# Kernel optimization log

Hardware: AMD Instinct MI355X
Metric: run time of the kernel (lower is better)

The kernel has to match this reference:

```python
import jax, jax.numpy as jnp
import numpy as np

TOPK = 2
SCALE = 32.0 / 16.0  # alpha / rank
EPS = 1e-20


def setup_inputs() -> dict:
    key = jax.random.key(0)
    ks = jax.random.split(key, 6)
    B, S, D = 4, 4096, 2048
    E, R, QO, VO = 8, 16, 2048, 2048
    return {
        "hidden_states": jax.random.normal(ks[0], (B, S, D), dtype=jnp.float32),
        "router_weight": jax.random.normal(ks[1], (E, D), dtype=jnp.float32) * 0.02,
        "q_lora_a": jax.random.normal(ks[2], (E, D, R), dtype=jnp.float32) * 0.02,
        "q_lora_b": jax.random.normal(ks[3], (E, R, QO), dtype=jnp.float32) * 0.02,
        "v_lora_a": jax.random.normal(ks[4], (E, D, R), dtype=jnp.float32) * 0.02,
        "v_lora_b": jax.random.normal(ks[5], (E, R, VO), dtype=jnp.float32) * 0.02,
    }


def reference(hidden_states, router_weight, q_lora_a, q_lora_b, v_lora_a, v_lora_b):
    orig_shape = hidden_states.shape[:-1]
    D = hidden_states.shape[-1]
    E = router_weight.shape[0]
    h = hidden_states.reshape(-1, D)                       # [T, D]

    # --- routing ---
    logits = h @ router_weight.T                           # [T, E]
    probs = jax.nn.softmax(logits, axis=-1)
    scores, idx = jax.lax.top_k(probs, TOPK)               # [T, K]
    scores = scores / (jnp.sum(scores, axis=-1, keepdims=True) + EPS)
    # dense per-expert combine weight (0 for unselected experts), incl. LoRA scale
    w = jnp.sum(jax.nn.one_hot(idx, E, dtype=h.dtype) * scores[..., None], axis=1) * SCALE  # [T, E]

    # --- grouped LoRA (dense over experts; E and rank are small) ---
    q_low = jnp.einsum('td,edr->ter', h, q_lora_a) * w[:, :, None]  # [T, E, R]
    v_low = jnp.einsum('td,edr->ter', h, v_lora_a) * w[:, :, None]
    q_delta = jnp.einsum('ter,erq->tq', q_low, q_lora_b)            # [T, QO]
    v_delta = jnp.einsum('ter,erv->tv', v_low, v_lora_b)            # [T, VO]

    return (q_delta.reshape(*orig_shape, q_delta.shape[-1]),
            v_delta.reshape(*orig_shape, v_delta.shape[-1]))
```

## Files before the change

### kernel.cpp

```cpp
#include <hip/hip_runtime.h>

#define T_TOKENS 16384
#define DIM 2048
#define NE 8
#define QOUT 2048
#define LSCALE 2.0f

typedef __attribute__((ext_vector_type(4))) float f32x4;
typedef __attribute__((ext_vector_type(8))) short s16x8;
typedef __attribute__((ext_vector_type(4))) short s16x4;

__device__ __forceinline__ short f2bf(float f) {
  unsigned u = __builtin_bit_cast(unsigned, f);
  u += 0x7fffu + ((u >> 16) & 1u);
  return (short)(u >> 16);
}

__global__ __launch_bounds__(256) void k_pack(
    const float* __restrict__ qa, const float* __restrict__ qb,
    const float* __restrict__ va, const float* __restrict__ vb,
    short* __restrict__ Bq1, short* __restrict__ Bv1,
    short* __restrict__ Bq2, short* __restrict__ Bv2) {
  int tid = blockIdx.x * 256 + threadIdx.x;
  if (tid < 65536) {
    int mat = tid >> 15;
    int idx = tid & 32767;
    int d8 = idx >> 7, c = idx & 127;
    int e = c >> 4, r = c & 15;
    const float* src = mat ? va : qa;
    short* dst = mat ? Bv1 : Bq1;
    s16x8 v;
#pragma unroll
    for (int j = 0; j < 8; ++j)
      v[j] = f2bf(src[((size_t)e * DIM + d8 * 8 + j) * 16 + r]);
    *(s16x8*)(dst + (size_t)idx * 8) = v;
  } else {
    int t2 = tid - 65536;
    int mat = t2 >> 15;
    int idx = t2 & 32767;
    int k8 = idx >> 11, c = idx & 2047;
    const float* src = mat ? vb : qb;
    short* dst = mat ? Bv2 : Bq2;
    s16x8 v;
#pragma unroll
    for (int j = 0; j < 8; ++j)
      v[j] = f2bf(src[(size_t)(k8 * 8 + j) * QOUT + c]);
    *(s16x8*)(dst + (size_t)idx * 8) = v;
  }
}

__global__ __launch_bounds__(256) void k_s1(
    const float* __restrict__ h, const float* __restrict__ rw,
    const short* __restrict__ Bq1, const short* __restrict__ Bv1,
    short* __restrict__ lowq, short* __restrict__ lowv) {
  __shared__ float rwl[NE * DIM];
  __shared__ short At[2][32][40];
  __shared__ float wl[32][NE];

  const int tid = threadIdx.x;
  const int lane = tid & 63, wv = tid >> 6;
  const int lrow = lane & 15, lk = lane >> 4;
  const int row0 = blockIdx.x * 32;
  const int c0 = wv * 64;
  const int r = tid >> 3;
  const int kq = (tid & 7) * 4;

  {
    const float4* src = (const float4*)rw;
    float4* dst = (float4*)rwl;
#pragma unroll
    for (int i = 0; i < 16; ++i) dst[tid + i * 256] = src[tid + i * 256];
  }
  __syncthreads();

  float lg[NE] = {0.f, 0.f, 0.f, 0.f, 0.f, 0.f, 0.f, 0.f};
  f32x4 acc[2][4] = {};
  int cur = 0;
  const float* hrow = h + (size_t)(row0 + r) * DIM + kq;

  for (int kb = 0; kb < DIM; kb += 32) {
    float4 hv = *(const float4*)(hrow + kb);
#pragma unroll
    for (int e = 0; e < NE; ++e) {
      float4 rv = *(const float4*)&rwl[e * DIM + kb + kq];
      lg[e] += hv.x * rv.x + hv.y * rv.y + hv.z * rv.z + hv.w * rv.w;
    }
    s16x4 hb4;
    hb4[0] = f2bf(hv.x); hb4[1] = f2bf(hv.y);
    hb4[2] = f2bf(hv.z); hb4[3] = f2bf(hv.w);
    *(s16x4*)&At[cur][r][kq] = hb4;
    s16x8 b[4];
#pragma unroll
    for (int ct = 0; ct < 4; ++ct) {
      int c = c0 + ct * 16 + lrow;
      int cc = c & 127;
      const short* bp = (c < 128) ? Bq1 : Bv1;
      b[ct] = *(const s16x8*)(bp + ((size_t)((kb >> 3) + lk) * 128 + cc) * 8);
    }
    __syncthreads();
    s16x8 a[2];
#pragma unroll
    for (int rt = 0; rt < 2; ++rt)
      a[rt] = *(const s16x8*)&At[cur][rt * 16 + lrow][lk * 8];
#pragma unroll
    for (int rt = 0; rt < 2; ++rt)
#pragma unroll
      for (int ct = 0; ct < 4; ++ct)
        acc[rt][ct] = __builtin_amdgcn_mfma_f32_16x16x32_bf16(b[ct], a[rt], acc[rt][ct], 0, 0, 0);
    cur ^= 1;
  }

#pragma unroll
  for (int e = 0; e < NE; ++e) {
    lg[e] += __shfl_xor(lg[e], 1, 64);
    lg[e] += __shfl_xor(lg[e], 2, 64);
    lg[e] += __shfl_xor(lg[e], 4, 64);
  }
  float mx = lg[0];
#pragma unroll
  for (int e = 1; e < NE; ++e) mx = fmaxf(mx, lg[e]);
  float p[NE], sum = 0.f;
#pragma unroll
  for (int e = 0; e < NE; ++e) { p[e] = expf(lg[e] - mx); sum += p[e]; }
  int i1 = 0; float v1 = p[0];
#pragma unroll
  for (int e = 1; e < NE; ++e) if (p[e] > v1) { v1 = p[e]; i1 = e; }
  float v2 = -1.f; int i2 = 0;
#pragma unroll
  for (int e = 0; e < NE; ++e) if (e != i1 && p[e] > v2) { v2 = p[e]; i2 = e; }
  float s1 = v1 / sum, s2 = v2 / sum;
  float dn = s1 + s2 + 1e-20f;
  float w1 = s1 / dn * LSCALE, w2 = s2 / dn * LSCALE;
  int el = tid & 7;
  wl[r][el] = (el == i1) ? w1 : ((el == i2) ? w2 : 0.f);
  __syncthreads();

#pragma unroll
  for (int rt = 0; rt < 2; ++rt)
#pragma unroll
    for (int ct = 0; ct < 4; ++ct) {
      int t = row0 + rt * 16 + lrow;
      int col = c0 + ct * 16 + lk * 4;
      int cc = col & 127;
      int e = cc >> 4;
      short* op = (col < 128) ? lowq : lowv;
      float wgt = wl[rt * 16 + lrow][e];
      s16x4 v;
#pragma unroll
      for (int j = 0; j < 4; ++j) v[j] = f2bf(acc[rt][ct][j] * wgt);
      *(s16x4*)(op + (size_t)t * 128 + cc) = v;
    }
}

__global__ __launch_bounds__(256) void k_up(
    const short* __restrict__ lowq, const short* __restrict__ lowv,
    const short* __restrict__ Bq2, const short* __restrict__ Bv2,
    float* __restrict__ out) {
  const int lane = threadIdx.x & 63, wv = threadIdx.x >> 6;
  const int lrow = lane & 15, lk = lane >> 4;
  const int row0 = blockIdx.x * 64;
  const int m = blockIdx.y >> 1;
  const int half = blockIdx.y & 1;
  const short* low = m ? lowv : lowq;
  const short* B = m ? Bv2 : Bq2;
  float* op = out + (size_t)m * T_TOKENS * QOUT;

  s16x8 a[4][4];
#pragma unroll
  for (int rt = 0; rt < 4; ++rt)
#pragma unroll
    for (int kk = 0; kk < 4; ++kk)
      a[rt][kk] = *(const s16x8*)(low + (size_t)(row0 + rt * 16 + lrow) * 128 + kk * 32 + lk * 8);

#pragma unroll
  for (int sub = 0; sub < 4; ++sub) {
    int cb = half * 1024 + sub * 256 + wv * 64;
    f32x4 acc[4][4] = {};
#pragma unroll
    for (int kk = 0; kk < 4; ++kk) {
      s16x8 b[4];
#pragma unroll
      for (int ct = 0; ct < 4; ++ct) {
        int c = cb + ct * 16 + lrow;
        b[ct] = *(const s16x8*)(B + ((size_t)(kk * 4 + lk) * QOUT + c) * 8);
      }
#pragma unroll
      for (int rt = 0; rt < 4; ++rt)
#pragma unroll
        for (int ct = 0; ct < 4; ++ct)
          acc[rt][ct] = __builtin_amdgcn_mfma_f32_16x16x32_bf16(b[ct], a[rt][kk], acc[rt][ct], 0, 0, 0);
    }
#pragma unroll
    for (int rt = 0; rt < 4; ++rt)
#pragma unroll
      for (int ct = 0; ct < 4; ++ct) {
        int t = row0 + rt * 16 + lrow;
        int col = cb + ct * 16 + lk * 4;
        *(f32x4*)(op + (size_t)t * QOUT + col) = acc[rt][ct];
      }
  }
}

extern "C" void kernel_launch(void* const* d_in, const int* in_sizes, int n_in,
                              void* d_out, int out_size, void* d_ws, size_t ws_size,
                              hipStream_t stream) {
  const float* h  = (const float*)d_in[0];
  const float* rw = (const float*)d_in[1];
  const float* qa = (const float*)d_in[2];
  const float* qb = (const float*)d_in[3];
  const float* va = (const float*)d_in[4];
  const float* vb = (const float*)d_in[5];
  float* out = (float*)d_out;
  char* ws = (char*)d_ws;

  short* Bq1 = (short*)(ws);
  short* Bv1 = (short*)(ws + (512 << 10));
  short* Bq2 = (short*)(ws + (1024 << 10));
  short* Bv2 = (short*)(ws + (1536 << 10));
  short* lowq = (short*)(ws + (2 << 20));
  short* lowv = (short*)(ws + (6 << 20));

  k_pack<<<512, 256, 0, stream>>>(qa, qb, va, vb, Bq1, Bv1, Bq2, Bv2);
  k_s1<<<T_TOKENS / 32, 256, 0, stream>>>(h, rw, Bq1, Bv1, lowq, lowv);
  dim3 g2(T_TOKENS / 64, 4);
  k_up<<<g2, 256, 0, stream>>>(lowq, lowv, Bq2, Bv2, out);
}
```

Baseline: 155.7 us.

## Prefetch next k-slice in s1, double tokens per block, tune k_up occupancy

The stage-1 kernel now processes 64 tokens per 512-thread block, so the router weights staged in LDS are reused across twice as many rows. Each iteration register-prefetches the next hidden-state and B1 fragments before the current MFMAs, and the full __syncthreads is replaced by an LDS-only waitcnt plus barrier. k_up gets a min-blocks-per-CU launch bound. The aim is to hide global-load latency and amortize the router-weight copy, at the cost of more registers and fewer resident blocks.

```diff
diff --git a/kernel.cpp b/kernel.cpp
--- a/kernel.cpp
+++ b/kernel.cpp
@@ -14,6 +14,11 @@
   unsigned u = __builtin_bit_cast(unsigned, f);
   u += 0x7fffu + ((u >> 16) & 1u);
   return (short)(u >> 16);
+}
+
+__device__ __forceinline__ void barrier_lds() {
+  asm volatile("s_waitcnt lgkmcnt(0)" ::: "memory");
+  __builtin_amdgcn_s_barrier();
 }
 
 __global__ __launch_bounds__(256) void k_pack(
@@ -49,19 +54,20 @@
   }
 }
 
-__global__ __launch_bounds__(256) void k_s1(
+__global__ __launch_bounds__(512, 4) void k_s1(
     const float* __restrict__ h, const float* __restrict__ rw,
     const short* __restrict__ Bq1, const short* __restrict__ Bv1,
     short* __restrict__ lowq, short* __restrict__ lowv) {
   __shared__ float rwl[NE * DIM];
-  __shared__ short At[2][32][40];
-  __shared__ float wl[32][NE];
+  __shared__ short At[2][64][40];
+  __shared__ float wl[64][NE];
 
   const int tid = threadIdx.x;
   const int lane = tid & 63, wv = tid >> 6;
   const int lrow = lane & 15, lk = lane >> 4;
-  const int row0 = blockIdx.x * 32;
-  const int c0 = wv * 64;
+  const int row0 = blockIdx.x * 64;
+  const int rh = wv >> 2;
+  const int c0 = (wv & 3) * 64;
   const int r = tid >> 3;
   const int kq = (tid & 7) * 4;
 
@@ -69,17 +75,36 @@
     const float4* src = (const float4*)rw;
     float4* dst = (float4*)rwl;
 #pragma unroll
-    for (int i = 0; i < 16; ++i) dst[tid + i * 256] = src[tid + i * 256];
+    for (int i = 0; i < 8; ++i) dst[tid + i * 512] = src[tid + i * 512];
   }
   __syncthreads();
+
+  const float* hrow = h + (size_t)(row0 + r) * DIM;
+  const short* bp[4]; int cc4[4];
+#pragma unroll
+  for (int ct = 0; ct < 4; ++ct) {
+    int c = c0 + ct * 16 + lrow;
+    bp[ct] = (c < 128) ? Bq1 : Bv1;
+    cc4[ct] = c & 127;
+  }
+
+  float4 hv = *(const float4*)(hrow + kq);
+  s16x8 b[4];
+#pragma unroll
+  for (int ct = 0; ct < 4; ++ct)
+    b[ct] = *(const s16x8*)(bp[ct] + ((size_t)lk * 128 + cc4[ct]) * 8);
 
   float lg[NE] = {0.f, 0.f, 0.f, 0.f, 0.f, 0.f, 0.f, 0.f};
   f32x4 acc[2][4] = {};
   int cur = 0;
-  const float* hrow = h + (size_t)(row0 + r) * DIM + kq;
 
   for (int kb = 0; kb < DIM; kb += 32) {
-    float4 hv = *(const float4*)(hrow + kb);
+    const int kn = (kb + 32) & (DIM - 1);
+    float4 hvn = *(const float4*)(hrow + kn + kq);
+    s16x8 bn[4];
+#pragma unroll
+    for (int ct = 0; ct < 4; ++ct)
+      bn[ct] = *(const s16x8*)(bp[ct] + ((size_t)((kn >> 3) + lk) * 128 + cc4[ct]) * 8);
 #pragma unroll
     for (int e = 0; e < NE; ++e) {
       float4 rv = *(const float4*)&rwl[e * DIM + kb + kq];
@@ -89,24 +114,19 @@
     hb4[0] = f2bf(hv.x); hb4[1] = f2bf(hv.y);
     hb4[2] = f2bf(hv.z); hb4[3] = f2bf(hv.w);
     *(s16x4*)&At[cur][r][kq] = hb4;
-    s16x8 b[4];
-#pragma unroll
-    for (int ct = 0; ct < 4; ++ct) {
-      int c = c0 + ct * 16 + lrow;
-      int cc = c & 127;
-      const short* bp = (c < 128) ? Bq1 : Bv1;
-      b[ct] = *(const s16x8*)(bp + ((size_t)((kb >> 3) + lk) * 128 + cc) * 8);
-    }
-    __syncthreads();
+    barrier_lds();
     s16x8 a[2];
 #pragma unroll
     for (int rt = 0; rt < 2; ++rt)
-      a[rt] = *(const s16x8*)&At[cur][rt * 16 + lrow][lk * 8];
+      a[rt] = *(const s16x8*)&At[cur][rh * 32 + rt * 16 + lrow][lk * 8];
 #pragma unroll
     for (int rt = 0; rt < 2; ++rt)
 #pragma unroll
       for (int ct = 0; ct < 4; ++ct)
         acc[rt][ct] = __builtin_amdgcn_mfma_f32_16x16x32_bf16(b[ct], a[rt], acc[rt][ct], 0, 0, 0);
+    hv = hvn;
+#pragma unroll
+    for (int ct = 0; ct < 4; ++ct) b[ct] = bn[ct];
     cur ^= 1;
   }
 
@@ -139,12 +159,13 @@
   for (int rt = 0; rt < 2; ++rt)
 #pragma unroll
     for (int ct = 0; ct < 4; ++ct) {
-      int t = row0 + rt * 16 + lrow;
+      int rr = rh * 32 + rt * 16 + lrow;
+      int t = row0 + rr;
       int col = c0 + ct * 16 + lk * 4;
       int cc = col & 127;
       int e = cc >> 4;
       short* op = (col < 128) ? lowq : lowv;
-      float wgt = wl[rt * 16 + lrow][e];
+      float wgt = wl[rr][e];
       s16x4 v;
 #pragma unroll
       for (int j = 0; j < 4; ++j) v[j] = f2bf(acc[rt][ct][j] * wgt);
@@ -152,7 +173,7 @@
     }
 }
 
-__global__ __launch_bounds__(256) void k_up(
+__global__ __launch_bounds__(256, 3) void k_up(
     const short* __restrict__ lowq, const short* __restrict__ lowv,
     const short* __restrict__ Bq2, const short* __restrict__ Bv2,
     float* __restrict__ out) {
@@ -221,7 +242,7 @@
   short* lowv = (short*)(ws + (6 << 20));
 
   k_pack<<<512, 256, 0, stream>>>(qa, qb, va, vb, Bq1, Bv1, Bq2, Bv2);
-  k_s1<<<T_TOKENS / 32, 256, 0, stream>>>(h, rw, Bq1, Bv1, lowq, lowv);
+  k_s1<<<T_TOKENS / 64, 512, 0, stream>>>(h, rw, Bq1, Bv1, lowq, lowv);
   dim3 g2(T_TOKENS / 64, 4);
   k_up<<<g2, 256, 0, stream>>>(lowq, lowv, Bq2, Bv2, out);
 }
```

Measured after the change: 143.1 us. 1.09x faster.

## Fuse down-projection, routing and up-projection into one kernel with LDS-resident low-rank tile

Applied to the files above, without the earlier changes.

Merges the stage-1 (router plus LoRA-A) kernel and the up-projection kernel into a single 512-thread kernel. The bf16 low-rank activations stay in LDS instead of making a global round trip. The router weights are now read from global/L2 rather than staged into LDS, and the h loads are prefetched two iterations ahead with a 64-wide K step. Output tiles are written with nontemporal stores and B2 fragments are software-pipelined. This removes one launch and the intermediate traffic, at the cost of higher register pressure and an up-projection spread over fewer blocks per token tile.

```diff
diff --git a/kernel.cpp b/kernel.cpp
--- a/kernel.cpp
+++ b/kernel.cpp
@@ -14,6 +14,11 @@
   unsigned u = __builtin_bit_cast(unsigned, f);
   u += 0x7fffu + ((u >> 16) & 1u);
   return (short)(u >> 16);
+}
+
+__device__ __forceinline__ void barrier_lds() {
+  asm volatile("s_waitcnt lgkmcnt(0)" ::: "memory");
+  __builtin_amdgcn_s_barrier();
 }
 
 __global__ __launch_bounds__(256) void k_pack(
@@ -49,65 +54,64 @@
   }
 }
 
-__global__ __launch_bounds__(256) void k_s1(
+__global__ __launch_bounds__(512, 4) void k_fused(
     const float* __restrict__ h, const float* __restrict__ rw,
     const short* __restrict__ Bq1, const short* __restrict__ Bv1,
-    short* __restrict__ lowq, short* __restrict__ lowv) {
-  __shared__ float rwl[NE * DIM];
-  __shared__ short At[2][32][40];
+    const short* __restrict__ Bq2, const short* __restrict__ Bv2,
+    float* __restrict__ out) {
+  __shared__ short At[2][32][72];
+  __shared__ short low[32][264];
   __shared__ float wl[32][NE];
 
   const int tid = threadIdx.x;
   const int lane = tid & 63, wv = tid >> 6;
   const int lrow = lane & 15, lk = lane >> 4;
   const int row0 = blockIdx.x * 32;
-  const int c0 = wv * 64;
-  const int r = tid >> 3;
-  const int kq = (tid & 7) * 4;
-
-  {
-    const float4* src = (const float4*)rw;
-    float4* dst = (float4*)rwl;
-#pragma unroll
-    for (int i = 0; i < 16; ++i) dst[tid + i * 256] = src[tid + i * 256];
-  }
-  __syncthreads();
+  const int r  = tid >> 4;
+  const int kq = (tid & 15) * 4;
+  const int tq = wv >> 2, cq = wv & 3;
+
+  const float* hrow = h + (size_t)(row0 + r) * DIM + kq;
+  const short* B1 = (cq >= 2) ? Bv1 : Bq1;
+  int cc4[4];
+#pragma unroll
+  for (int ct = 0; ct < 4; ++ct) cc4[ct] = (cq & 1) * 64 + ct * 16 + lrow;
+
+  float4 hv0 = *(const float4*)(hrow);
+  float4 hv1 = *(const float4*)(hrow + 64);
 
   float lg[NE] = {0.f, 0.f, 0.f, 0.f, 0.f, 0.f, 0.f, 0.f};
-  f32x4 acc[2][4] = {};
-  int cur = 0;
-  const float* hrow = h + (size_t)(row0 + r) * DIM + kq;
-
-  for (int kb = 0; kb < DIM; kb += 32) {
-    float4 hv = *(const float4*)(hrow + kb);
+  f32x4 acc1[4] = {};
+
+  for (int kb = 0; kb < DIM; kb += 64) {
+    const int cur = (kb >> 6) & 1;
+    float4 hv2 = *(const float4*)(hrow + ((kb + 128) & (DIM - 1)));
+    s16x8 bA[4], bB[4];
+#pragma unroll
+    for (int ct = 0; ct < 4; ++ct) {
+      int d8 = (kb >> 3) + lk;
+      bA[ct] = *(const s16x8*)(B1 + ((size_t)d8 * 128 + cc4[ct]) * 8);
+      bB[ct] = *(const s16x8*)(B1 + ((size_t)(d8 + 4) * 128 + cc4[ct]) * 8);
+    }
+    s16x4 hb4;
+    hb4[0] = f2bf(hv0.x); hb4[1] = f2bf(hv0.y);
+    hb4[2] = f2bf(hv0.z); hb4[3] = f2bf(hv0.w);
+    *(s16x4*)&At[cur][r][kq] = hb4;
 #pragma unroll
     for (int e = 0; e < NE; ++e) {
-      float4 rv = *(const float4*)&rwl[e * DIM + kb + kq];
-      lg[e] += hv.x * rv.x + hv.y * rv.y + hv.z * rv.z + hv.w * rv.w;
-    }
-    s16x4 hb4;
-    hb4[0] = f2bf(hv.x); hb4[1] = f2bf(hv.y);
-    hb4[2] = f2bf(hv.z); hb4[3] = f2bf(hv.w);
-    *(s16x4*)&At[cur][r][kq] = hb4;
-    s16x8 b[4];
-#pragma unroll
-    for (int ct = 0; ct < 4; ++ct) {
-      int c = c0 + ct * 16 + lrow;
-      int cc = c & 127;
-      const short* bp = (c < 128) ? Bq1 : Bv1;
-      b[ct] = *(const s16x8*)(bp + ((size_t)((kb >> 3) + lk) * 128 + cc) * 8);
-    }
-    __syncthreads();
-    s16x8 a[2];
-#pragma unroll
-    for (int rt = 0; rt < 2; ++rt)
-      a[rt] = *(const s16x8*)&At[cur][rt * 16 + lrow][lk * 8];
-#pragma unroll
-    for (int rt = 0; rt < 2; ++rt)
-#pragma unroll
-      for (int ct = 0; ct < 4; ++ct)
-        acc[rt][ct] = __builtin_amdgcn_mfma_f32_16x16x32_bf16(b[ct], a[rt], acc[rt][ct], 0, 0, 0);
-    cur ^= 1;
+      float4 rv = *(const float4*)(rw + e * DIM + kb + kq);
+      lg[e] += hv0.x * rv.x + hv0.y * rv.y + hv0.z * rv.z + hv0.w * rv.w;
+    }
+    barrier_lds();
+    s16x8 a0 = *(const s16x8*)&At[cur][tq * 16 + lrow][lk * 8];
+    s16x8 a1 = *(const s16x8*)&At[cur][tq * 16 + lrow][32 + lk * 8];
+#pragma unroll
+    for (int ct = 0; ct < 4; ++ct)
+      acc1[ct] = __builtin_amdgcn_mfma_f32_16x16x32_bf16(bA[ct], a0, acc1[ct], 0, 0, 0);
+#pragma unroll
+    for (int ct = 0; ct < 4; ++ct)
+      acc1[ct] = __builtin_amdgcn_mfma_f32_16x16x32_bf16(bB[ct], a1, acc1[ct], 0, 0, 0);
+    hv0 = hv1; hv1 = hv2;
   }
 
 #pragma unroll
@@ -115,6 +119,7 @@
     lg[e] += __shfl_xor(lg[e], 1, 64);
     lg[e] += __shfl_xor(lg[e], 2, 64);
     lg[e] += __shfl_xor(lg[e], 4, 64);
+    lg[e] += __shfl_xor(lg[e], 8, 64);
   }
   float mx = lg[0];
 #pragma unroll
@@ -131,73 +136,73 @@
   float s1 = v1 / sum, s2 = v2 / sum;
   float dn = s1 + s2 + 1e-20f;
   float w1 = s1 / dn * LSCALE, w2 = s2 / dn * LSCALE;
-  int el = tid & 7;
-  wl[r][el] = (el == i1) ? w1 : ((el == i2) ? w2 : 0.f);
+  if ((tid & 15) < 8) {
+    int el = tid & 7;
+    wl[r][el] = (el == i1) ? w1 : ((el == i2) ? w2 : 0.f);
+  }
+
+  const int m = wv >> 2;
+  const int cwave = (wv & 3) * 512;
+  const short* B2 = m ? Bv2 : Bq2;
+  s16x8 bc[4];
+#pragma unroll
+  for (int ct = 0; ct < 4; ++ct) {
+    int c = cwave + ct * 16 + lrow;
+    bc[ct] = *(const s16x8*)(B2 + ((size_t)lk * QOUT + c) * 8);
+  }
+
   __syncthreads();
-
+  float wgt[4];
+#pragma unroll
+  for (int ct = 0; ct < 4; ++ct) wgt[ct] = wl[tq * 16 + lrow][(cq & 1) * 4 + ct];
+#pragma unroll
+  for (int ct = 0; ct < 4; ++ct) {
+    s16x4 v;
+#pragma unroll
+    for (int j = 0; j < 4; ++j) v[j] = f2bf(acc1[ct][j] * wgt[ct]);
+    *(s16x4*)&low[tq * 16 + lrow][cq * 64 + ct * 16 + lk * 4] = v;
+  }
+  barrier_lds();
+
+  float* op = out + (size_t)m * T_TOKENS * QOUT;
+  s16x8 a2[2][4];
 #pragma unroll
   for (int rt = 0; rt < 2; ++rt)
 #pragma unroll
+    for (int kk = 0; kk < 4; ++kk)
+      a2[rt][kk] = *(const s16x8*)&low[rt * 16 + lrow][m * 128 + kk * 32 + lk * 8];
+
+  f32x4 acc[2][4] = {};
+#pragma unroll
+  for (int it = 0; it < 32; ++it) {
+    const int sub = it >> 2, kk = it & 3;
+    const int itn = (it + 1) & 31;
+    const int subn = itn >> 2, kkn = itn & 3;
+    s16x8 bn[4];
+#pragma unroll
     for (int ct = 0; ct < 4; ++ct) {
-      int t = row0 + rt * 16 + lrow;
-      int col = c0 + ct * 16 + lk * 4;
-      int cc = col & 127;
-      int e = cc >> 4;
-      short* op = (col < 128) ? lowq : lowv;
-      float wgt = wl[rt * 16 + lrow][e];
-      s16x4 v;
-#pragma unroll
-      for (int j = 0; j < 4; ++j) v[j] = f2bf(acc[rt][ct][j] * wgt);
-      *(s16x4*)(op + (size_t)t * 128 + cc) = v;
-    }
-}
-
-__global__ __launch_bounds__(256) void k_up(
-    const short* __restrict__ lowq, const short* __restrict__ lowv,
-    const short* __restrict__ Bq2, const short* __restrict__ Bv2,
-    float* __restrict__ out) {
-  const int lane = threadIdx.x & 63, wv = threadIdx.x >> 6;
-  const int lrow = lane & 15, lk = lane >> 4;
-  const int row0 = blockIdx.x * 64;
-  const int m = blockIdx.y >> 1;
-  const int half = blockIdx.y & 1;
-  const short* low = m ? lowv : lowq;
-  const short* B = m ? Bv2 : Bq2;
-  float* op = out + (size_t)m * T_TOKENS * QOUT;
-
-  s16x8 a[4][4];
-#pragma unroll
-  for (int rt = 0; rt < 4; ++rt)
-#pragma unroll
-    for (int kk = 0; kk < 4; ++kk)
-      a[rt][kk] = *(const s16x8*)(low + (size_t)(row0 + rt * 16 + lrow) * 128 + kk * 32 + lk * 8);
-
-#pragma unroll
-  for (int sub = 0; sub < 4; ++sub) {
-    int cb = half * 1024 + sub * 256 + wv * 64;
-    f32x4 acc[4][4] = {};
-#pragma unroll
-    for (int kk = 0; kk < 4; ++kk) {
-      s16x8 b[4];
-#pragma unroll
-      for (int ct = 0; ct < 4; ++ct) {
-        int c = cb + ct * 16 + lrow;
-        b[ct] = *(const s16x8*)(B + ((size_t)(kk * 4 + lk) * QOUT + c) * 8);
-      }
-#pragma unroll
-      for (int rt = 0; rt < 4; ++rt)
-#pragma unroll
-        for (int ct = 0; ct < 4; ++ct)
-          acc[rt][ct] = __builtin_amdgcn_mfma_f32_16x16x32_bf16(b[ct], a[rt][kk], acc[rt][ct], 0, 0, 0);
-    }
-#pragma unroll
-    for (int rt = 0; rt < 4; ++rt)
-#pragma unroll
-      for (int ct = 0; ct < 4; ++ct) {
-        int t = row0 + rt * 16 + lrow;
-        int col = cb + ct * 16 + lk * 4;
-        *(f32x4*)(op + (size_t)t * QOUT + col) = acc[rt][ct];
-      }
+      int c = cwave + subn * 64 + ct * 16 + lrow;
+      bn[ct] = *(const s16x8*)(B2 + ((size_t)(kkn * 4 + lk) * QOUT + c) * 8);
+    }
+#pragma unroll
+    for (int rt = 0; rt < 2; ++rt)
+#pragma unroll
+      for (int ct = 0; ct < 4; ++ct)
+        acc[rt][ct] = __builtin_amdgcn_mfma_f32_16x16x32_bf16(bc[ct], a2[rt][kk], acc[rt][ct], 0, 0, 0);
+    if (kk == 3) {
+      int cb = cwave + sub * 64;
+#pragma unroll
+      for (int rt = 0; rt < 2; ++rt)
+#pragma unroll
+        for (int ct = 0; ct < 4; ++ct) {
+          int t = row0 + rt * 16 + lrow;
+          int col = cb + ct * 16 + lk * 4;
+          __builtin_nontemporal_store(acc[rt][ct], (f32x4*)(op + (size_t)t * QOUT + col));
+          acc[rt][ct] = (f32x4){0.f, 0.f, 0.f, 0.f};
+        }
+    }
+#pragma unroll
+    for (int ct = 0; ct < 4; ++ct) bc[ct] = bn[ct];
   }
 }
 
@@ -217,11 +222,7 @@
   short* Bv1 = (short*)(ws + (512 << 10));
   short* Bq2 = (short*)(ws + (1024 << 10));
   short* Bv2 = (short*)(ws + (1536 << 10));
-  short* lowq = (short*)(ws + (2 << 20));
-  short* lowv = (short*)(ws + (6 << 20));
 
   k_pack<<<512, 256, 0, stream>>>(qa, qb, va, vb, Bq1, Bv1, Bq2, Bv2);
-  k_s1<<<T_TOKENS / 32, 256, 0, stream>>>(h, rw, Bq1, Bv1, lowq, lowv);
-  dim3 g2(T_TOKENS / 64, 4);
-  k_up<<<g2, 256, 0, stream>>>(lowq, lowv, Bq2, Bv2, out);
-}
+  k_fused<<<T_TOKENS / 32, 512, 0, stream>>>(h, rw, Bq1, Bv1, Bq2, Bv2, out);
+}
```

Measured after the change: 163.3 us. 1.05x slower.
